# Kernel optimization log

Hardware: AMD Instinct MI355X
Metric: run time of the kernel (lower is better)

Reference implementation:

```python
import jax, jax.numpy as jnp
import numpy as np

STRIDE = 1

def setup_inputs() -> dict:
    key = jax.random.key(0)
    k1, k2 = jax.random.split(key)
    x = jax.random.normal(k1, (16, 32, 32768), dtype=jnp.float32)
    # original uses torch.rand -> uniform [0,1)
    kernel = jax.random.uniform(k2, (1, 32, 32, 3), dtype=jnp.float32)
    return {"x": x, "kernel": kernel}

def reference(x, kernel):
    # Faithful intent of the module: strided valid 1D convolution.
    # x: (B, C_in, L); kernel: (1, C_out, C_in, K)
    w = kernel[0]  # (C_out, C_in, K)
    out = jax.lax.conv_general_dilated(
        x, w,
        window_strides=(STRIDE,),
        padding='VALID',
        dimension_numbers=('NCH', 'OIH', 'NCH'),
    )  # (B, C_out, (L-K)//STRIDE + 1)
    return out
```

## Files before the change

kernel.cpp:

```cpp
#include <hip/hip_runtime.h>

#define L_IN   32768
#define L_OUT  32766
#define C_IN   32
#define C_OUT  32
#define KW     3
#define TILE_L 128
#define NTILES 256
#define PITCH  40
#define XROWS  (TILE_L + 2)

typedef __attribute__((ext_vector_type(8))) short bf16x8;
typedef __attribute__((ext_vector_type(4))) float f32x4;

__device__ __forceinline__ unsigned short bf16_rne(float f) {
    unsigned u = __float_as_uint(f);
    u += 0x7fffu + ((u >> 16) & 1u);
    return (unsigned short)(u >> 16);
}
__device__ __forceinline__ float bf16_to_f32(unsigned short h) {
    return __uint_as_float(((unsigned)h) << 16);
}

__global__ void prep_w(const float* __restrict__ w, unsigned short* __restrict__ wtf) {
    const int i = blockIdx.x * 256 + threadIdx.x;
    if (i >= 6 * 64 * 8) return;
    const int f    = i >> 9;
    const int rr   = i & 511;
    const int lane = rr >> 3;
    const int j    = rr & 7;
    const int kw   = f >> 1;
    const int cot  = f & 1;
    const int co   = cot * 16 + (lane & 15);
    const int ci   = (lane >> 4) * 8 + j;
    const float v  = w[(co * C_IN + ci) * KW + kw];
    const unsigned short hi = bf16_rne(v);
    const unsigned short lo = bf16_rne(v - bf16_to_f32(hi));
    wtf[(f * 64 + lane) * 16 + j]     = hi;
    wtf[(f * 64 + lane) * 16 + 8 + j] = lo;
}

__global__ __launch_bounds__(256, 4) void conv1d_mfma(
    const float* __restrict__ x, const unsigned short* __restrict__ wtf,
    float* __restrict__ out)
{
    __shared__ __attribute__((aligned(16))) unsigned short xh[XROWS * PITCH];
    __shared__ __attribute__((aligned(16))) unsigned short xl[XROWS * PITCH];

    const int tid  = threadIdx.x;
    const int lane = tid & 63;
    const int wv   = tid >> 6;
    const int bb   = blockIdx.x >> 8;
    const int tile = blockIdx.x & (NTILES - 1);
    const int l0   = tile * TILE_L;

    const float* xb = x + ((size_t)bb * C_IN) * L_IN + l0;

    bf16x8 wah[6], wal[6];
#pragma unroll
    for (int f = 0; f < 6; ++f) {
        const bf16x8* p = (const bf16x8*)(wtf + (f * 64 + lane) * 16);
        wah[f] = p[0];
        wal[f] = p[1];
    }

    {
        const int c    = tid & 31;
        const int rrow = tid >> 5;
#pragma unroll
        for (int r = 0; r < 4; ++r) {
            const int ci = rrow + r * 8;
            const float* src = xb + (size_t)ci * L_IN;
#pragma unroll
            for (int q = 0; q < 4; ++q) {
                const int l = c + q * 32;
                const float v = src[l];
                const unsigned short hi = bf16_rne(v);
                const unsigned short lo = bf16_rne(v - bf16_to_f32(hi));
                xh[l * PITCH + ci] = hi;
                xl[l * PITCH + ci] = lo;
            }
        }
    }
    if (tid < 64) {
        const int h  = tid & 1;
        const int ci = tid >> 1;
        const int gl = l0 + TILE_L + h;
        float v = 0.f;
        if (gl < L_IN) v = xb[(size_t)ci * L_IN + TILE_L + h];
        const unsigned short hi = bf16_rne(v);
        const unsigned short lo = bf16_rne(v - bf16_to_f32(hi));
        xh[(TILE_L + h) * PITCH + ci] = hi;
        xl[(TILE_L + h) * PITCH + ci] = lo;
    }
    __syncthreads();

    const int n  = lane & 15;
    const int kg = lane >> 4;
    const int lb = wv * 32;

    f32x4 acc[2][2] = {{{0.f,0.f,0.f,0.f},{0.f,0.f,0.f,0.f}},
                       {{0.f,0.f,0.f,0.f},{0.f,0.f,0.f,0.f}}};

#pragma unroll
    for (int kw = 0; kw < KW; ++kw) {
#pragma unroll
        for (int lt = 0; lt < 2; ++lt) {
            const int lrow = lb + lt * 16 + n + kw;
            const bf16x8 bh = *(const bf16x8*)&xh[lrow * PITCH + kg * 8];
            const bf16x8 bl = *(const bf16x8*)&xl[lrow * PITCH + kg * 8];
#pragma unroll
            for (int cot = 0; cot < 2; ++cot) {
                const int f = kw * 2 + cot;
                acc[cot][lt] = __builtin_amdgcn_mfma_f32_16x16x32_bf16(wah[f], bh, acc[cot][lt], 0, 0, 0);
                acc[cot][lt] = __builtin_amdgcn_mfma_f32_16x16x32_bf16(wah[f], bl, acc[cot][lt], 0, 0, 0);
                acc[cot][lt] = __builtin_amdgcn_mfma_f32_16x16x32_bf16(wal[f], bh, acc[cot][lt], 0, 0, 0);
            }
        }
    }

    float* ob = out + (size_t)bb * C_OUT * L_OUT;
    const int lw = l0 + lb;
#pragma unroll
    for (int cot = 0; cot < 2; ++cot) {
#pragma unroll
        for (int lt = 0; lt < 2; ++lt) {
            const int l = lw + lt * 16 + n;
            if (l < L_OUT) {
                float* op = ob + (size_t)(cot * 16 + kg * 4) * L_OUT + l;
#pragma unroll
                for (int r = 0; r < 4; ++r)
                    op[(size_t)r * L_OUT] = acc[cot][lt][r];
            }
        }
    }
}

extern "C" void kernel_launch(void* const* d_in, const int* in_sizes, int n_in,
                              void* d_out, int out_size, void* d_ws, size_t ws_size,
                              hipStream_t stream) {
    const float* x = (const float*)d_in[0];
    const float* w = (const float*)d_in[1];
    float* out     = (float*)d_out;
    unsigned short* wtf = (unsigned short*)d_ws;

    prep_w<<<dim3(12), 256, 0, stream>>>(w, wtf);
    conv1d_mfma<<<dim3(16 * NTILES), 256, 0, stream>>>(x, wtf, out);
}
```

Before: 126.5 us.

## Process four tiles per block with double-buffered LDS prefetch and swizzled packed layout

Each block now handles four consecutive 128-wide tiles, prefetching the next tile's global loads into registers while computing the current one and writing them into a second LDS buffer. The hi/lo bf16 split is packed into one 32-bit word per element in an XOR-swizzled LDS layout, and the halves are unpacked with bit operations before the MFMAs. The lo part is now truncated instead of rounded, and the fast store path skips per-element bounds checks. This amortizes weight loads and launch overhead and overlaps memory with compute, at the cost of fewer blocks (1024) and more registers and ALU work per tile.

```diff
diff --git a/kernel.cpp b/kernel.cpp
--- a/kernel.cpp
+++ b/kernel.cpp
@@ -6,20 +6,26 @@
 #define C_OUT  32
 #define KW     3
 #define TILE_L 128
-#define NTILES 256
-#define PITCH  40
-#define XROWS  (TILE_L + 2)
+#define TPB    4
+#define XROWS  130
+#define PITCHW 32
+#define LDSW   (XROWS * PITCHW)
 
 typedef __attribute__((ext_vector_type(8))) short bf16x8;
 typedef __attribute__((ext_vector_type(4))) float f32x4;
-
-__device__ __forceinline__ unsigned short bf16_rne(float f) {
-    unsigned u = __float_as_uint(f);
-    u += 0x7fffu + ((u >> 16) & 1u);
-    return (unsigned short)(u >> 16);
-}
-__device__ __forceinline__ float bf16_to_f32(unsigned short h) {
-    return __uint_as_float(((unsigned)h) << 16);
+typedef __attribute__((ext_vector_type(4))) unsigned int u32x4;
+
+#define PIN(v_) asm volatile("" : "+v"(v_))
+
+__device__ __forceinline__ unsigned pack_split(float v) {
+    unsigned u = __float_as_uint(v);
+    unsigned r = u + 0x7fffu + ((u >> 16) & 1u);
+    float lo = v - __uint_as_float(r & 0xffff0000u);
+    return (__float_as_uint(lo) & 0xffff0000u) | (r >> 16);
+}
+
+__device__ __forceinline__ int lds_word(int l, int ci) {
+    return l * PITCHW + ((((ci >> 2) ^ (l & 7)) << 2) | (ci & 3));
 }
 
 __global__ void prep_w(const float* __restrict__ w, unsigned short* __restrict__ wtf) {
@@ -34,8 +40,13 @@
     const int co   = cot * 16 + (lane & 15);
     const int ci   = (lane >> 4) * 8 + j;
     const float v  = w[(co * C_IN + ci) * KW + kw];
-    const unsigned short hi = bf16_rne(v);
-    const unsigned short lo = bf16_rne(v - bf16_to_f32(hi));
+    unsigned u = __float_as_uint(v);
+    unsigned r = u + 0x7fffu + ((u >> 16) & 1u);
+    unsigned short hi = (unsigned short)(r >> 16);
+    float lof = v - __uint_as_float(r & 0xffff0000u);
+    unsigned lu = __float_as_uint(lof);
+    unsigned lr = lu + 0x7fffu + ((lu >> 16) & 1u);
+    unsigned short lo = (unsigned short)(lr >> 16);
     wtf[(f * 64 + lane) * 16 + j]     = hi;
     wtf[(f * 64 + lane) * 16 + 8 + j] = lo;
 }
@@ -44,94 +55,139 @@
     const float* __restrict__ x, const unsigned short* __restrict__ wtf,
     float* __restrict__ out)
 {
-    __shared__ __attribute__((aligned(16))) unsigned short xh[XROWS * PITCH];
-    __shared__ __attribute__((aligned(16))) unsigned short xl[XROWS * PITCH];
+    __shared__ __attribute__((aligned(16))) unsigned xp[2][LDSW];
 
     const int tid  = threadIdx.x;
     const int lane = tid & 63;
     const int wv   = tid >> 6;
-    const int bb   = blockIdx.x >> 8;
-    const int tile = blockIdx.x & (NTILES - 1);
-    const int l0   = tile * TILE_L;
-
-    const float* xb = x + ((size_t)bb * C_IN) * L_IN + l0;
-
-    bf16x8 wah[6], wal[6];
+    const int bb   = blockIdx.x >> 6;
+    const int grp  = blockIdx.x & 63;
+    const int lg0  = grp * (TILE_L * TPB);
+
+    const float* xb = x + (size_t)bb * C_IN * L_IN;
+
+    u32x4 wah[6], wal[6];
 #pragma unroll
     for (int f = 0; f < 6; ++f) {
-        const bf16x8* p = (const bf16x8*)(wtf + (f * 64 + lane) * 16);
+        const u32x4* p = (const u32x4*)(wtf + (f * 64 + lane) * 16);
         wah[f] = p[0];
         wal[f] = p[1];
     }
 
-    {
-        const int c    = tid & 31;
-        const int rrow = tid >> 5;
+    const int c   = tid & 31;
+    const int rr0 = tid >> 5;
+    const int n   = lane & 15;
+    const int kg  = lane >> 4;
+    const int lb  = wv * 32;
+
+    float sv[4][4];
+    float hv;
+
+    auto LOADT = [&](int l0) {
 #pragma unroll
         for (int r = 0; r < 4; ++r) {
-            const int ci = rrow + r * 8;
-            const float* src = xb + (size_t)ci * L_IN;
-#pragma unroll
-            for (int q = 0; q < 4; ++q) {
-                const int l = c + q * 32;
-                const float v = src[l];
-                const unsigned short hi = bf16_rne(v);
-                const unsigned short lo = bf16_rne(v - bf16_to_f32(hi));
-                xh[l * PITCH + ci] = hi;
-                xl[l * PITCH + ci] = lo;
+            const float* src = xb + (size_t)(rr0 + r * 8) * L_IN + l0;
+#pragma unroll
+            for (int q = 0; q < 4; ++q)
+                sv[r][q] = src[c + q * 32];
+        }
+        hv = 0.f;
+        if (tid < 64) {
+            const int gl = l0 + TILE_L + (tid & 1);
+            if (gl < L_IN) hv = xb[(size_t)(tid >> 1) * L_IN + gl];
+        }
+        asm volatile("" ::: "memory");
+    };
+    auto WRITET = [&](int buf) {
+        unsigned* xs = xp[buf];
+#pragma unroll
+        for (int r = 0; r < 4; ++r)
+#pragma unroll
+            for (int q = 0; q < 4; ++q)
+                xs[lds_word(c + q * 32, rr0 + r * 8)] = pack_split(sv[r][q]);
+        if (tid < 64)
+            xs[lds_word(TILE_L + (tid & 1), tid >> 1)] = pack_split(hv);
+    };
+
+    LOADT(lg0);
+    WRITET(0);
+#pragma unroll
+    for (int f = 0; f < 6; ++f) { PIN(wah[f]); PIN(wal[f]); }
+
+    float* ob = out + (size_t)bb * C_OUT * L_OUT;
+
+#pragma unroll
+    for (int t = 0; t < TPB; ++t) {
+        const int l0 = lg0 + t * TILE_L;
+        if (t + 1 < TPB) LOADT(l0 + TILE_L);
+        __syncthreads();
+
+        const unsigned* xs = xp[t & 1];
+        f32x4 acc[2][2];
+#pragma unroll
+        for (int a = 0; a < 2; ++a)
+#pragma unroll
+            for (int bq = 0; bq < 2; ++bq)
+                acc[a][bq] = (f32x4){0.f, 0.f, 0.f, 0.f};
+
+#pragma unroll
+        for (int kw = 0; kw < KW; ++kw) {
+#pragma unroll
+            for (int lt = 0; lt < 2; ++lt) {
+                const int lrow = lb + lt * 16 + n + kw;
+                const int base = lrow * PITCHW;
+                const int sw   = lrow & 7;
+                const u32x4 pa = *(const u32x4*)&xs[base + (((kg * 2 + 0) ^ sw) << 2)];
+                const u32x4 pb = *(const u32x4*)&xs[base + (((kg * 2 + 1) ^ sw) << 2)];
+                u32x4 BH, BL;
+                BH[0] = (pa[0] & 0xffffu) | (pa[1] << 16);
+                BH[1] = (pa[2] & 0xffffu) | (pa[3] << 16);
+                BH[2] = (pb[0] & 0xffffu) | (pb[1] << 16);
+                BH[3] = (pb[2] & 0xffffu) | (pb[3] << 16);
+                BL[0] = (pa[0] >> 16) | (pa[1] & 0xffff0000u);
+                BL[1] = (pa[2] >> 16) | (pa[3] & 0xffff0000u);
+                BL[2] = (pb[0] >> 16) | (pb[1] & 0xffff0000u);
+                BL[3] = (pb[2] >> 16) | (pb[3] & 0xffff0000u);
+                const bf16x8 bh = __builtin_bit_cast(bf16x8, BH);
+                const bf16x8 bl = __builtin_bit_cast(bf16x8, BL);
+#pragma unroll
+                for (int cot = 0; cot < 2; ++cot) {
+                    const int f = kw * 2 + cot;
+                    const bf16x8 ah = __builtin_bit_cast(bf16x8, wah[f]);
+                    const bf16x8 al = __builtin_bit_cast(bf16x8, wal[f]);
+                    acc[cot][lt] = __builtin_amdgcn_mfma_f32_16x16x32_bf16(ah, bh, acc[cot][lt], 0, 0, 0);
+                    acc[cot][lt] = __builtin_amdgcn_mfma_f32_16x16x32_bf16(ah, bl, acc[cot][lt], 0, 0, 0);
+                    acc[cot][lt] = __builtin_amdgcn_mfma_f32_16x16x32_bf16(al, bh, acc[cot][lt], 0, 0, 0);
+                }
             }
         }
-    }
-    if (tid < 64) {
-        const int h  = tid & 1;
-        const int ci = tid >> 1;
-        const int gl = l0 + TILE_L + h;
-        float v = 0.f;
-        if (gl < L_IN) v = xb[(size_t)ci * L_IN + TILE_L + h];
-        const unsigned short hi = bf16_rne(v);
-        const unsigned short lo = bf16_rne(v - bf16_to_f32(hi));
-        xh[(TILE_L + h) * PITCH + ci] = hi;
-        xl[(TILE_L + h) * PITCH + ci] = lo;
-    }
-    __syncthreads();
-
-    const int n  = lane & 15;
-    const int kg = lane >> 4;
-    const int lb = wv * 32;
-
-    f32x4 acc[2][2] = {{{0.f,0.f,0.f,0.f},{0.f,0.f,0.f,0.f}},
-                       {{0.f,0.f,0.f,0.f},{0.f,0.f,0.f,0.f}}};
-
-#pragma unroll
-    for (int kw = 0; kw < KW; ++kw) {
-#pragma unroll
-        for (int lt = 0; lt < 2; ++lt) {
-            const int lrow = lb + lt * 16 + n + kw;
-            const bf16x8 bh = *(const bf16x8*)&xh[lrow * PITCH + kg * 8];
-            const bf16x8 bl = *(const bf16x8*)&xl[lrow * PITCH + kg * 8];
-#pragma unroll
-            for (int cot = 0; cot < 2; ++cot) {
-                const int f = kw * 2 + cot;
-                acc[cot][lt] = __builtin_amdgcn_mfma_f32_16x16x32_bf16(wah[f], bh, acc[cot][lt], 0, 0, 0);
-                acc[cot][lt] = __builtin_amdgcn_mfma_f32_16x16x32_bf16(wah[f], bl, acc[cot][lt], 0, 0, 0);
-                acc[cot][lt] = __builtin_amdgcn_mfma_f32_16x16x32_bf16(wal[f], bh, acc[cot][lt], 0, 0, 0);
-            }
-        }
-    }
-
-    float* ob = out + (size_t)bb * C_OUT * L_OUT;
-    const int lw = l0 + lb;
-#pragma unroll
-    for (int cot = 0; cot < 2; ++cot) {
-#pragma unroll
-        for (int lt = 0; lt < 2; ++lt) {
-            const int l = lw + lt * 16 + n;
-            if (l < L_OUT) {
-                float* op = ob + (size_t)(cot * 16 + kg * 4) * L_OUT + l;
-#pragma unroll
-                for (int r = 0; r < 4; ++r)
-                    op[(size_t)r * L_OUT] = acc[cot][lt][r];
-            }
+
+        if (t + 1 < TPB) WRITET((t + 1) & 1);
+
+        const int lw = l0 + lb;
+        if (lw + 31 < L_OUT) {
+#pragma unroll
+            for (int cot = 0; cot < 2; ++cot)
+#pragma unroll
+                for (int lt = 0; lt < 2; ++lt) {
+                    float* op = ob + (size_t)(cot * 16 + kg * 4) * L_OUT + lw + lt * 16 + n;
+#pragma unroll
+                    for (int r = 0; r < 4; ++r)
+                        op[(size_t)r * L_OUT] = acc[cot][lt][r];
+                }
+        } else {
+#pragma unroll
+            for (int cot = 0; cot < 2; ++cot)
+#pragma unroll
+                for (int lt = 0; lt < 2; ++lt) {
+                    const int l = lw + lt * 16 + n;
+                    if (l < L_OUT) {
+                        float* op = ob + (size_t)(cot * 16 + kg * 4) * L_OUT + l;
+#pragma unroll
+                        for (int r = 0; r < 4; ++r)
+                            op[(size_t)r * L_OUT] = acc[cot][lt][r];
+                    }
+                }
         }
     }
 }
@@ -145,5 +201,5 @@
     unsigned short* wtf = (unsigned short*)d_ws;
 
     prep_w<<<dim3(12), 256, 0, stream>>>(w, wtf);
-    conv1d_mfma<<<dim3(16 * NTILES), 256, 0, stream>>>(x, wtf, out);
-}
+    conv1d_mfma<<<dim3(16 * 64), 256, 0, stream>>>(x, wtf, out);
+}
```

After: 127.8 us. Within noise of the previous version (+1.0%).
